# Optimization experiments

Hardware: AMD Instinct MI355X
Metric: run time of the kernel (lower is better)

The kernel has to match this reference:

```python
import jax, jax.numpy as jnp
import numpy as np

N_TARGETS = 21
R_HW = 7
FM_H, FM_W = 64, 64
N_ROIS = 300


def setup_inputs() -> dict:
    key = jax.random.key(0)
    k1, k2, k3, k4 = jax.random.split(key, 4)
    FM = jax.random.normal(k1, (N_TARGETS * R_HW ** 2, FM_H, FM_W), dtype=jnp.float32)
    # Build valid ROIs (x1, y1, x2, y2) in feature-map pixel coordinates.
    x1 = jax.random.uniform(k2, (N_ROIS,), minval=0.0, maxval=FM_W * 0.6)
    y1 = jax.random.uniform(k3, (N_ROIS,), minval=0.0, maxval=FM_H * 0.6)
    wh = jax.random.uniform(k4, (N_ROIS, 2), minval=R_HW, maxval=FM_W * 0.4)
    x2 = jnp.minimum(x1 + wh[:, 0], FM_W - 1.0)
    y2 = jnp.minimum(y1 + wh[:, 1], FM_H - 1.0)
    rois = jnp.stack([x1, y1, x2, y2], axis=1).astype(jnp.float32)
    return {"FM": FM, "rois": rois, "n_targets": N_TARGETS, "r_hw": R_HW}


def _bin_masks(start, length, r_hw, size, dtype):
    """start, length: [R]; returns [R, r_hw, size] float bin-membership masks."""
    p = jnp.arange(r_hw, dtype=dtype)
    bin_sz = length / r_hw  # [R]
    lo = jnp.floor(start[:, None] + p[None, :] * bin_sz[:, None])          # [R, r_hw]
    hi = jnp.ceil(start[:, None] + (p[None, :] + 1.0) * bin_sz[:, None])   # [R, r_hw]
    lo = jnp.clip(lo, 0.0, size)
    hi = jnp.clip(hi, 0.0, size)
    idx = jnp.arange(size, dtype=dtype)
    mask = (idx[None, None, :] >= lo[:, :, None]) & (idx[None, None, :] < hi[:, :, None])
    return mask.astype(dtype)


def reference(FM, rois, n_targets, r_hw):
    """Position-sensitive ROI pooling (R-FCN).
    FM: [n_targets*r_hw^2, H, W]; rois: [R, 4] as (x1, y1, x2, y2).
    Returns pooled: [R, n_targets, r_hw, r_hw].
    Bin (p, q) of target t averages FM channel t*r_hw^2 + p*r_hw + q over the
    pixels in that bin; empty bins yield 0.
    """
    C, H, W = FM.shape
    dtype = FM.dtype
    FMr = FM.reshape(n_targets, r_hw, r_hw, H, W)  # [t, p, q, h, w]
    x1, y1, x2, y2 = rois[:, 0], rois[:, 1], rois[:, 2], rois[:, 3]
    roi_h = jnp.maximum(y2 - y1, 0.1)
    roi_w = jnp.maximum(x2 - x1, 0.1)
    mask_h = _bin_masks(y1, roi_h, r_hw, H, dtype)  # [R, p, H]
    mask_w = _bin_masks(x1, roi_w, r_hw, W, dtype)  # [R, q, W]
    # Sum over w per output column q, then over h per output row p.
    tmp = jnp.einsum('tpqhw,rqw->rtpqh', FMr, mask_w)
    s = jnp.einsum('rtpqh,rph->rtpq', tmp, mask_h)
    cnt = mask_h.sum(-1)[:, None, :, None] * mask_w.sum(-1)[:, None, None, :]  # [R,1,p,q]
    return s / jnp.maximum(cnt, 1.0)
```

## Files before the change

kernel.cpp:

```cpp
#include <hip/hip_runtime.h>


#define N_TARGETS 21
#define R_HW 7
#define FM_H 64
#define FM_W 64
#define PLANE (FM_H * FM_W)
#define CPT (N_TARGETS * R_HW * R_HW)

__global__ __launch_bounds__(256) void psroi_kernel(
    const float* __restrict__ FM,
    const float* __restrict__ rois,
    float* __restrict__ out,
    int n_rois) {
  __shared__ float sm[PLANE];

  const int c   = blockIdx.x;
  const int tid = threadIdx.x;

  const float* __restrict__ plane = FM + (size_t)c * PLANE;
#pragma unroll
  for (int i = 0; i < 4; ++i) {
    int off = (i * 256 + tid) * 4;
    *reinterpret_cast<float4*>(&sm[off]) =
        *reinterpret_cast<const float4*>(plane + off);
  }

  const int pq = c % (R_HW * R_HW);
  const int p  = pq / R_HW;
  const int q  = pq % R_HW;

  __syncthreads();

  for (int r = tid; r < n_rois; r += 256) {
    const float4 rv = reinterpret_cast<const float4*>(rois)[r];
    const float x1 = rv.x, y1 = rv.y, x2 = rv.z, y2 = rv.w;

    const float bw = fmaxf(x2 - x1, 0.1f) / (float)R_HW;
    const float bh = fmaxf(y2 - y1, 0.1f) / (float)R_HW;

    float lo_wf = fminf(fmaxf(floorf(x1 + (float)q * bw), 0.0f), (float)FM_W);
    float hi_wf = fminf(fmaxf(ceilf (x1 + ((float)q + 1.0f) * bw), 0.0f), (float)FM_W);
    float lo_hf = fminf(fmaxf(floorf(y1 + (float)p * bh), 0.0f), (float)FM_H);
    float hi_hf = fminf(fmaxf(ceilf (y1 + ((float)p + 1.0f) * bh), 0.0f), (float)FM_H);

    const int w0 = (int)lo_wf, w1 = (int)hi_wf;
    const int h0 = (int)lo_hf, h1 = (int)hi_hf;
    const int cnt = max(h1 - h0, 0) * max(w1 - w0, 0);

    const int a  = min(w0 & ~3, FM_W - 4);
    const int a2 = min(a + 4,   FM_W - 4);

    float s = 0.0f;
#pragma unroll
    for (int i = 0; i < 5; ++i) {
      const int h  = h0 + i;
      const int hc = min(h, FM_H - 1);
      const bool hin = (h < h1);
      const float* __restrict__ row = &sm[hc * FM_W];
      const float4 v0 = *reinterpret_cast<const float4*>(row + a);
      const float4 v1 = *reinterpret_cast<const float4*>(row + a2);

      float rs = 0.0f;
      int w;
      w = a + 0;  rs += (w >= w0 && w < w1) ? v0.x : 0.0f;
      w = a + 1;  rs += (w >= w0 && w < w1) ? v0.y : 0.0f;
      w = a + 2;  rs += (w >= w0 && w < w1) ? v0.z : 0.0f;
      w = a + 3;  rs += (w >= w0 && w < w1) ? v0.w : 0.0f;
      w = a + 4;  rs += (w >= w0 && w < w1) ? v1.x : 0.0f;
      w = a + 5;  rs += (w >= w0 && w < w1) ? v1.y : 0.0f;
      w = a + 6;  rs += (w >= w0 && w < w1) ? v1.z : 0.0f;
      w = a + 7;  rs += (w >= w0 && w < w1) ? v1.w : 0.0f;

      s += hin ? rs : 0.0f;
    }

    out[(size_t)r * CPT + c] = s / (float)(cnt > 0 ? cnt : 1);
  }
}

extern "C" void kernel_launch(void* const* d_in, const int* in_sizes, int n_in,
                              void* d_out, int out_size, void* d_ws, size_t ws_size,
                              hipStream_t stream) {
  const float* FM   = (const float*)d_in[0];
  const float* rois = (const float*)d_in[1];
  float* out = (float*)d_out;

  int n_rois = in_sizes[1] / 4;

  psroi_kernel<<<CPT, 256, 0, stream>>>(FM, rois, out, n_rois);
}
```

Baseline: 71.49 us.

## Load feature plane directly into LDS and precompute ROI bins before barrier

The plane copy now uses the AMD direct global-to-LDS load builtin instead of going through registers. Per-ROI bin bounds and reciprocal counts are computed into registers before the barrier, so that ROI math overlaps with the in-flight plane load. The final division becomes a multiply by a precomputed reciprocal. The kernel now handles at most 512 ROIs per launch, and correctness depends on the compiler inserting the right wait before the barrier for the async LDS loads.

```diff
diff --git a/kernel.cpp b/kernel.cpp
--- a/kernel.cpp
+++ b/kernel.cpp
@@ -7,6 +7,10 @@
 #define FM_W 64
 #define PLANE (FM_H * FM_W)
 #define CPT (N_TARGETS * R_HW * R_HW)
+#define MAX_ROI_PER_THREAD 2
+
+typedef __attribute__((address_space(3))) float lds_f32;
+typedef __attribute__((address_space(1))) const float glb_f32;
 
 __global__ __launch_bounds__(256) void psroi_kernel(
     const float* __restrict__ FM,
@@ -21,35 +25,58 @@
   const float* __restrict__ plane = FM + (size_t)c * PLANE;
 #pragma unroll
   for (int i = 0; i < 4; ++i) {
-    int off = (i * 256 + tid) * 4;
-    *reinterpret_cast<float4*>(&sm[off]) =
-        *reinterpret_cast<const float4*>(plane + off);
+    const int off = (i * 256 + tid) * 4;
+    __builtin_amdgcn_global_load_lds((glb_f32*)(plane + off),
+                                     (lds_f32*)(&sm[off]),
+                                     16, 0, 0);
   }
 
   const int pq = c % (R_HW * R_HW);
   const int p  = pq / R_HW;
   const int q  = pq % R_HW;
 
+  int g_w0[MAX_ROI_PER_THREAD], g_w1[MAX_ROI_PER_THREAD];
+  int g_h0[MAX_ROI_PER_THREAD], g_h1[MAX_ROI_PER_THREAD];
+  int g_a[MAX_ROI_PER_THREAD];
+  float g_inv[MAX_ROI_PER_THREAD];
+  int nmine = 0;
+
+#pragma unroll
+  for (int j = 0; j < MAX_ROI_PER_THREAD; ++j) {
+    const int r = tid + j * 256;
+    if (r < n_rois) {
+      const float4 rv = reinterpret_cast<const float4*>(rois)[r];
+      const float x1 = rv.x, y1 = rv.y, x2 = rv.z, y2 = rv.w;
+
+      const float bw = fmaxf(x2 - x1, 0.1f) / (float)R_HW;
+      const float bh = fmaxf(y2 - y1, 0.1f) / (float)R_HW;
+
+      const float lo_wf = fminf(fmaxf(floorf(x1 + (float)q * bw), 0.0f), (float)FM_W);
+      const float hi_wf = fminf(fmaxf(ceilf (x1 + ((float)q + 1.0f) * bw), 0.0f), (float)FM_W);
+      const float lo_hf = fminf(fmaxf(floorf(y1 + (float)p * bh), 0.0f), (float)FM_H);
+      const float hi_hf = fminf(fmaxf(ceilf (y1 + ((float)p + 1.0f) * bh), 0.0f), (float)FM_H);
+
+      const int w0 = (int)lo_wf, w1 = (int)hi_wf;
+      const int h0 = (int)lo_hf, h1 = (int)hi_hf;
+      const int cnt = max(h1 - h0, 0) * max(w1 - w0, 0);
+
+      g_w0[j] = w0;
+      g_w1[j] = w1;
+      g_h0[j] = h0;
+      g_h1[j] = h1;
+      g_a[j]  = min(w0 & ~3, FM_W - 4);
+      g_inv[j] = 1.0f / (float)(cnt > 0 ? cnt : 1);
+      nmine = j + 1;
+    }
+  }
+
   __syncthreads();
 
-  for (int r = tid; r < n_rois; r += 256) {
-    const float4 rv = reinterpret_cast<const float4*>(rois)[r];
-    const float x1 = rv.x, y1 = rv.y, x2 = rv.z, y2 = rv.w;
-
-    const float bw = fmaxf(x2 - x1, 0.1f) / (float)R_HW;
-    const float bh = fmaxf(y2 - y1, 0.1f) / (float)R_HW;
-
-    float lo_wf = fminf(fmaxf(floorf(x1 + (float)q * bw), 0.0f), (float)FM_W);
-    float hi_wf = fminf(fmaxf(ceilf (x1 + ((float)q + 1.0f) * bw), 0.0f), (float)FM_W);
-    float lo_hf = fminf(fmaxf(floorf(y1 + (float)p * bh), 0.0f), (float)FM_H);
-    float hi_hf = fminf(fmaxf(ceilf (y1 + ((float)p + 1.0f) * bh), 0.0f), (float)FM_H);
-
-    const int w0 = (int)lo_wf, w1 = (int)hi_wf;
-    const int h0 = (int)lo_hf, h1 = (int)hi_hf;
-    const int cnt = max(h1 - h0, 0) * max(w1 - w0, 0);
-
-    const int a  = min(w0 & ~3, FM_W - 4);
-    const int a2 = min(a + 4,   FM_W - 4);
+  for (int j = 0; j < nmine; ++j) {
+    const int w0 = g_w0[j], w1 = g_w1[j];
+    const int h0 = g_h0[j], h1 = g_h1[j];
+    const int a  = g_a[j];
+    const int a2 = min(a + 4, FM_W - 4);
 
     float s = 0.0f;
 #pragma unroll
@@ -75,7 +102,8 @@
       s += hin ? rs : 0.0f;
     }
 
-    out[(size_t)r * CPT + c] = s / (float)(cnt > 0 ? cnt : 1);
+    const int r = tid + j * 256;
+    out[(size_t)r * CPT + c] = s * g_inv[j];
   }
 }
 
```

New measurement: 70.69 us. No clear change (-1.1%).
